# Optimization experiments

Hardware: AMD Instinct MI355X
Metric: run time of the kernel (lower is better)

The kernel has to match this reference:

```python
import jax, jax.numpy as jnp
import numpy as np

N = 100000      # nodes
E = 1600000     # edges (avg degree 16)
DIN = 512
DOUT = 64
NEG_SLOPE = 0.2


def spmm(rows, cols, vals, x, n):
    # sparse [n,n] (COO) @ dense [n,d]: out[r] += vals[e] * x[cols[e]]
    return jax.ops.segment_sum(vals[:, None] * x[cols], rows, num_segments=n)


def setup_inputs() -> dict:
    key = jax.random.key(0)
    k1, k2, k3, k4, k5 = jax.random.split(key, 5)
    features = jax.random.normal(k1, (N, DIN), dtype=jnp.float32)
    edge_rows = jax.random.randint(k2, (E,), 0, N, dtype=jnp.int32)
    edge_cols = jax.random.randint(k3, (E,), 0, N, dtype=jnp.int32)
    edge_vals = jax.random.uniform(k4, (E,), dtype=jnp.float32)
    limit = float(np.sqrt(6.0 / (DIN + DOUT)))  # xavier_uniform
    weight = jax.random.uniform(k5, (DIN, DOUT), dtype=jnp.float32,
                                minval=-limit, maxval=limit)
    return {"features": features, "weight": weight,
            "edge_rows": edge_rows, "edge_cols": edge_cols,
            "edge_vals": edge_vals}


def reference(features, weight, edge_rows, edge_cols, edge_vals):
    # active=True path: fused dense mm + LeakyReLU(0.2)
    support = jax.nn.leaky_relu(features @ weight, negative_slope=NEG_SLOPE)
    output = spmm(edge_rows, edge_cols, edge_vals, support, N)  # adj @ support
    az = spmm(edge_rows, edge_cols, edge_vals, output, N)       # adj @ output
    return (output, az)
```

## Files before the change

kernel.cpp:

```cpp
#include <hip/hip_runtime.h>
#include <hip/hip_bf16.h>

#define DIN 512
#define DOUT 64

typedef float float4v __attribute__((ext_vector_type(4)));

__global__ __launch_bounds__(256) void gemm_lrelu_kernel(
    const float* __restrict__ X, const float* __restrict__ W,
    float* __restrict__ sup, int N)
{
  const int t    = threadIdx.x;
  const int wave = t >> 6;
  const int lane = t & 63;
  const int h = __builtin_amdgcn_readfirstlane((wave & 1) * 32);
  const int row  = blockIdx.x * 128 + (wave >> 1) * 64 + lane;
  const int rowr = row < N ? row : N - 1;

  float acc[32];
#pragma unroll
  for (int c = 0; c < 32; ++c) acc[c] = 0.0f;

  const float* __restrict__ xrow = X + (size_t)rowr * DIN;

#pragma unroll 1
  for (int k = 0; k < DIN; k += 4) {
    const float4v xv = *reinterpret_cast<const float4v*>(xrow + k);
#pragma unroll
    for (int kk = 0; kk < 4; ++kk) {
      const float* __restrict__ wk = W + (k + kk) * DOUT + h;
      const float xs = xv[kk];
#pragma unroll
      for (int c = 0; c < 32; ++c) acc[c] = fmaf(wk[c], xs, acc[c]);
    }
  }

  if (row < N) {
    float* __restrict__ o = sup + (size_t)row * DOUT + h;
#pragma unroll
    for (int c = 0; c < 32; ++c) {
      const float v = acc[c];
      o[c] = v > 0.0f ? v : 0.2f * v;
    }
  }
}

__global__ __launch_bounds__(256) void hist_kernel(
    const int* __restrict__ er, int* __restrict__ cnt, int E)
{
  int i = blockIdx.x * blockDim.x + threadIdx.x;
  const int stride = gridDim.x * blockDim.x;
  for (; i < E; i += stride) atomicAdd(&cnt[er[i]], 1);
}

__global__ __launch_bounds__(256) void scan_block_kernel(
    const int* __restrict__ in, int* __restrict__ out,
    int* __restrict__ bsum, int n)
{
  __shared__ int s[256];
  const int t = threadIdx.x;
  const int gid = blockIdx.x * 256 + t;
  const int v = gid < n ? in[gid] : 0;
  s[t] = v;
  __syncthreads();
#pragma unroll
  for (int off = 1; off < 256; off <<= 1) {
    const int add = t >= off ? s[t - off] : 0;
    __syncthreads();
    s[t] += add;
    __syncthreads();
  }
  if (gid < n) out[gid] = s[t] - v;
  if (t == 255) bsum[blockIdx.x] = s[255];
}

__global__ __launch_bounds__(256) void scan_bsums_kernel(int* __restrict__ bsum, int nb)
{
  __shared__ int s[256];
  __shared__ int carry_s;
  const int t = threadIdx.x;
  if (t == 0) carry_s = 0;
  __syncthreads();
  for (int base = 0; base < nb; base += 256) {
    const int i = base + t;
    const int v = i < nb ? bsum[i] : 0;
    s[t] = v;
    __syncthreads();
#pragma unroll
    for (int off = 1; off < 256; off <<= 1) {
      const int add = t >= off ? s[t - off] : 0;
      __syncthreads();
      s[t] += add;
      __syncthreads();
    }
    const int carry = carry_s;
    if (i < nb) bsum[i] = s[t] - v + carry;
    const int total = s[255];
    __syncthreads();
    if (t == 0) carry_s = carry + total;
    __syncthreads();
  }
}

__global__ __launch_bounds__(256) void scan_add_kernel(
    int* __restrict__ out, const int* __restrict__ bsum, int n)
{
  const int gid = blockIdx.x * 256 + threadIdx.x;
  if (gid < n) out[gid] += bsum[blockIdx.x];
}

__global__ __launch_bounds__(256) void scatter_kernel(
    const int* __restrict__ er, const int* __restrict__ ec,
    const float* __restrict__ ev, int* __restrict__ cursor,
    int* __restrict__ scols, float* __restrict__ svals, int E)
{
  int i = blockIdx.x * blockDim.x + threadIdx.x;
  const int stride = gridDim.x * blockDim.x;
  for (; i < E; i += stride) {
    const int r = er[i];
    const int pos = atomicAdd(&cursor[r], 1);
    scols[pos] = ec[i];
    svals[pos] = ev[i];
  }
}

__global__ __launch_bounds__(256) void spmm_csr_kernel(
    const int* __restrict__ rowptr, const int* __restrict__ scols,
    const float* __restrict__ svals, const float* __restrict__ x,
    float* __restrict__ out, int N)
{
  const int lane = threadIdx.x & 63;
  const int row  = blockIdx.x * 4 + (threadIdx.x >> 6);
  if (row >= N) return;

  const int s = rowptr[row];
  const int e = rowptr[row + 1];
  float acc = 0.0f;

  int i = s;
  for (; i + 4 <= e; i += 4) {
    const int b = __builtin_amdgcn_readfirstlane(i);
    const int c0 = scols[b],     c1 = scols[b + 1];
    const int c2 = scols[b + 2], c3 = scols[b + 3];
    const float v0 = svals[b],     v1 = svals[b + 1];
    const float v2 = svals[b + 2], v3 = svals[b + 3];
    const float x0 = x[(size_t)c0 * DOUT + lane];
    const float x1 = x[(size_t)c1 * DOUT + lane];
    const float x2 = x[(size_t)c2 * DOUT + lane];
    const float x3 = x[(size_t)c3 * DOUT + lane];
    acc = fmaf(v0, x0, acc);
    acc = fmaf(v1, x1, acc);
    acc = fmaf(v2, x2, acc);
    acc = fmaf(v3, x3, acc);
  }
  for (; i < e; ++i) {
    const int b = __builtin_amdgcn_readfirstlane(i);
    acc = fmaf(svals[b], x[(size_t)scols[b] * DOUT + lane], acc);
  }

  out[(size_t)row * DOUT + lane] = acc;
}

extern "C" void kernel_launch(void* const* d_in, const int* in_sizes, int n_in,
                              void* d_out, int out_size, void* d_ws, size_t ws_size,
                              hipStream_t stream)
{
  const float* X  = (const float*)d_in[0];
  const float* W  = (const float*)d_in[1];
  const int*   er = (const int*)d_in[2];
  const int*   ec = (const int*)d_in[3];
  const float* ev = (const float*)d_in[4];

  const int N = in_sizes[0] / DIN;
  const int E = in_sizes[2];
  const size_t half = (size_t)N * DOUT;

  char* w = (char*)d_ws;
  float* sup    = (float*)w;                 w += half * sizeof(float);
  int*   rowptr = (int*)w;                   w += (size_t)(N + 1) * sizeof(int);
  int*   cursor = (int*)w;                   w += (size_t)(N + 1) * sizeof(int);
  int*   bsum   = (int*)w;                   w += 1024 * sizeof(int);
  int*   scols  = (int*)w;                   w += (size_t)E * sizeof(int);
  float* svals  = (float*)w;

  float* out0 = (float*)d_out;
  float* out1 = out0 + half;

  const int n_scan = N + 1;
  const int nb = (n_scan + 255) / 256;

  hipMemsetAsync(cursor, 0, (size_t)n_scan * sizeof(int), stream);
  hist_kernel<<<2048, 256, 0, stream>>>(er, cursor, E);
  scan_block_kernel<<<nb, 256, 0, stream>>>(cursor, rowptr, bsum, n_scan);
  scan_bsums_kernel<<<1, 256, 0, stream>>>(bsum, nb);
  scan_add_kernel<<<nb, 256, 0, stream>>>(rowptr, bsum, n_scan);
  hipMemcpyAsync(cursor, rowptr, (size_t)n_scan * sizeof(int),
                 hipMemcpyDeviceToDevice, stream);
  scatter_kernel<<<2048, 256, 0, stream>>>(er, ec, ev, cursor, scols, svals, E);

  gemm_lrelu_kernel<<<(N + 127) / 128, 256, 0, stream>>>(X, W, sup, N);

  spmm_csr_kernel<<<(N + 3) / 4, 256, 0, stream>>>(rowptr, scols, svals, sup, out0, N);
  spmm_csr_kernel<<<(N + 3) / 4, 256, 0, stream>>>(rowptr, scols, svals, out0, out1, N);
}
```

Before: 445.1 us.

## Replace scalar FMA GEMM with fp16 MFMA kernel staging weights in LDS

Rewrites the dense X@W + LeakyReLU step to use 16x16x32 f16 MFMA instructions. Inputs are converted to fp16 on the fly and weights are packed into shared memory in two K halves. The old kernel was a scalar-FMA loop that rereads W from global memory for every row. This trades fp32 accuracy for fp16 products with fp32 accumulation, and each block now reloads and converts W into LDS.

Result: faster. 388.0 us (-12.8%).

```diff
diff --git a/kernel.cpp b/kernel.cpp
--- a/kernel.cpp
+++ b/kernel.cpp
@@ -5,42 +5,88 @@
 #define DOUT 64
 
 typedef float float4v __attribute__((ext_vector_type(4)));
-
-__global__ __launch_bounds__(256) void gemm_lrelu_kernel(
+typedef float f32x4 __attribute__((ext_vector_type(4)));
+typedef _Float16 f16x8 __attribute__((ext_vector_type(8)));
+typedef unsigned int uint4v __attribute__((ext_vector_type(4)));
+
+static __device__ __forceinline__ unsigned int pk_f16(float a, float b) {
+  return __builtin_bit_cast(unsigned int, __builtin_amdgcn_cvt_pkrtz(a, b));
+}
+
+__global__ __launch_bounds__(256) void gemm_mfma_kernel(
     const float* __restrict__ X, const float* __restrict__ W,
     float* __restrict__ sup, int N)
 {
+  __shared__ unsigned int wlds[128][68];
+
   const int t    = threadIdx.x;
-  const int wave = t >> 6;
+  const int wv   = t >> 6;
   const int lane = t & 63;
-  const int h = __builtin_amdgcn_readfirstlane((wave & 1) * 32);
-  const int row  = blockIdx.x * 128 + (wave >> 1) * 64 + lane;
-  const int rowr = row < N ? row : N - 1;
-
-  float acc[32];
-#pragma unroll
-  for (int c = 0; c < 32; ++c) acc[c] = 0.0f;
-
-  const float* __restrict__ xrow = X + (size_t)rowr * DIN;
+  const int l15  = lane & 15;
+  const int g    = lane >> 4;
+
+  const int rb   = blockIdx.x * 64 + wv * 16;
+  const int rA   = rb + l15;
+  const int rowA = rA < N ? rA : N - 1;
+  const float* __restrict__ xrow = X + (size_t)rowA * DIN;
+
+  f32x4 acc[4];
+#pragma unroll
+  for (int f = 0; f < 4; ++f) acc[f] = (f32x4)0.0f;
 
 #pragma unroll 1
-  for (int k = 0; k < DIN; k += 4) {
-    const float4v xv = *reinterpret_cast<const float4v*>(xrow + k);
-#pragma unroll
-    for (int kk = 0; kk < 4; ++kk) {
-      const float* __restrict__ wk = W + (k + kk) * DOUT + h;
-      const float xs = xv[kk];
-#pragma unroll
-      for (int c = 0; c < 32; ++c) acc[c] = fmaf(wk[c], xs, acc[c]);
-    }
-  }
-
-  if (row < N) {
-    float* __restrict__ o = sup + (size_t)row * DOUT + h;
-#pragma unroll
-    for (int c = 0; c < 32; ++c) {
-      const float v = acc[c];
-      o[c] = v > 0.0f ? v : 0.2f * v;
+  for (int kh = 0; kh < 2; ++kh) {
+    const int kbase = kh * 256;
+    __syncthreads();
+#pragma unroll
+    for (int i = 0; i < 32; ++i) {
+      const int idx = t + i * 256;
+      const int c = idx & 63;
+      const int p = idx >> 6;
+      const float w0 = W[(size_t)(kbase + 2 * p) * DOUT + c];
+      const float w1 = W[(size_t)(kbase + 2 * p + 1) * DOUT + c];
+      wlds[p][c] = pk_f16(w0, w1);
+    }
+    __syncthreads();
+
+#pragma unroll
+    for (int s = 0; s < 8; ++s) {
+      const int k0 = kbase + s * 32;
+      const f32x4 a0 = *reinterpret_cast<const f32x4*>(xrow + k0 + g * 8);
+      const f32x4 a1 = *reinterpret_cast<const f32x4*>(xrow + k0 + g * 8 + 4);
+      uint4v au;
+      au[0] = pk_f16(a0[0], a0[1]);
+      au[1] = pk_f16(a0[2], a0[3]);
+      au[2] = pk_f16(a1[0], a1[1]);
+      au[3] = pk_f16(a1[2], a1[3]);
+      const f16x8 afrag = __builtin_bit_cast(f16x8, au);
+
+      const int pb = s * 16 + g * 4;
+#pragma unroll
+      for (int f = 0; f < 4; ++f) {
+        const int c = f * 16 + l15;
+        uint4v bu;
+        bu[0] = wlds[pb + 0][c];
+        bu[1] = wlds[pb + 1][c];
+        bu[2] = wlds[pb + 2][c];
+        bu[3] = wlds[pb + 3][c];
+        const f16x8 bfrag = __builtin_bit_cast(f16x8, bu);
+        acc[f] = __builtin_amdgcn_mfma_f32_16x16x32_f16(afrag, bfrag, acc[f], 0, 0, 0);
+      }
+    }
+  }
+
+  const int r0 = rb + g * 4;
+#pragma unroll
+  for (int f = 0; f < 4; ++f) {
+    const int c = f * 16 + l15;
+#pragma unroll
+    for (int reg = 0; reg < 4; ++reg) {
+      const int r = r0 + reg;
+      if (r < N) {
+        const float v = acc[f][reg];
+        sup[(size_t)r * DOUT + c] = v > 0.0f ? v : 0.2f * v;
+      }
     }
   }
 }
@@ -189,16 +235,16 @@
   const int n_scan = N + 1;
   const int nb = (n_scan + 255) / 256;
 
-  hipMemsetAsync(cursor, 0, (size_t)n_scan * sizeof(int), stream);
+  (void)hipMemsetAsync(cursor, 0, (size_t)n_scan * sizeof(int), stream);
   hist_kernel<<<2048, 256, 0, stream>>>(er, cursor, E);
   scan_block_kernel<<<nb, 256, 0, stream>>>(cursor, rowptr, bsum, n_scan);
   scan_bsums_kernel<<<1, 256, 0, stream>>>(bsum, nb);
   scan_add_kernel<<<nb, 256, 0, stream>>>(rowptr, bsum, n_scan);
-  hipMemcpyAsync(cursor, rowptr, (size_t)n_scan * sizeof(int),
-                 hipMemcpyDeviceToDevice, stream);
+  (void)hipMemcpyAsync(cursor, rowptr, (size_t)n_scan * sizeof(int),
+                       hipMemcpyDeviceToDevice, stream);
   scatter_kernel<<<2048, 256, 0, stream>>>(er, ec, ev, cursor, scols, svals, E);
 
-  gemm_lrelu_kernel<<<(N + 127) / 128, 256, 0, stream>>>(X, W, sup, N);
+  gemm_mfma_kernel<<<(N + 63) / 64, 256, 0, stream>>>(X, W, sup, N);
 
   spmm_csr_kernel<<<(N + 3) / 4, 256, 0, stream>>>(rowptr, scols, svals, sup, out0, N);
   spmm_csr_kernel<<<(N + 3) / 4, 256, 0, stream>>>(rowptr, scols, svals, out0, out1, N);
```
